# Optimization experiments

Hardware: AMD Instinct MI355X
Metric: run time of the kernel (lower is better)

The kernel has to match this reference:

```python
import jax, jax.numpy as jnp
import numpy as np

N_NODES = 100000
N_EDGES = 1600000
IN_F, HID, EMB = 128, 64, 32


def setup_inputs() -> dict:
    key = jax.random.key(0)
    ks = jax.random.split(key, 10)
    x = jax.random.normal(ks[0], (N_NODES, IN_F), dtype=jnp.float32)
    edge_index = jax.random.randint(ks[1], (2, N_EDGES), 0, N_NODES, dtype=jnp.int64)
    s = lambda k, sh, fan_in: jax.random.normal(k, sh, dtype=jnp.float32) / jnp.sqrt(jnp.float32(fan_in))
    return {
        "x": x,
        "edge_index": edge_index,
        # SAGEConv1: lin_l (applied to aggregated neighbors, with bias) + lin_r (root, no bias)
        "W1_l": s(ks[2], (IN_F, HID), IN_F), "b1": jnp.zeros((HID,), jnp.float32), "W1_r": s(ks[3], (IN_F, HID), IN_F),
        # SAGEConv2
        "W2_l": s(ks[4], (HID, EMB), HID), "b2": jnp.zeros((EMB,), jnp.float32), "W2_r": s(ks[5], (HID, EMB), HID),
        # risk head
        "Wh": s(ks[6], (EMB, 1), EMB), "bh": jnp.zeros((1,), jnp.float32),
    }


def _sage_conv(x, src, dst, W_l, b, W_r):
    # gather messages from source nodes, segment-mean at destination nodes
    msg_sum = jax.ops.segment_sum(x[src], dst, num_segments=N_NODES)  # [N, F]
    cnt = jax.ops.segment_sum(jnp.ones((src.shape[0],), x.dtype), dst, num_segments=N_NODES)
    mean_agg = msg_sum / jnp.maximum(cnt, 1.0)[:, None]  # isolated nodes -> 0
    return mean_agg @ W_l + b + x @ W_r


def reference(x, edge_index, W1_l, b1, W1_r, W2_l, b2, W2_r, Wh, bh):
    src, dst = edge_index[0], edge_index[1]
    h = jax.nn.relu(_sage_conv(x, src, dst, W1_l, b1, W1_r))
    # dropout is identity in eval mode
    embeddings = jax.nn.relu(_sage_conv(h, src, dst, W2_l, b2, W2_r))
    risk_scores = embeddings @ Wh + bh
    return embeddings, risk_scores
```

## Files before the change

### kernel.cpp

```cpp
#include <hip/hip_runtime.h>
#include <hip/hip_bf16.h>

#define N_NODES 100000
#define N_EDGES 1600000
#define NBUCK   196
#define BSHIFT  9
#define BCAP    12288

typedef __bf16 bf16x8 __attribute__((ext_vector_type(8)));
typedef float  f32x4  __attribute__((ext_vector_type(4)));
typedef float  f32x2  __attribute__((ext_vector_type(2)));


__device__ inline unsigned char enc_fp8(float v) {
    return (unsigned char)(__builtin_amdgcn_cvt_pk_fp8_f32(v, v, 0, 0) & 0xFF);
}

__global__ __launch_bounds__(256) void partition_k(const int* __restrict__ ei,
                                                   int* __restrict__ gcur,
                                                   unsigned* __restrict__ bbuf) {
    __shared__ int hist[NBUCK];
    __shared__ int cur[NBUCK];
    int t = threadIdx.x;
    for (int i = t; i < NBUCK; i += 256) hist[i] = 0;
    __syncthreads();
    int base = blockIdx.x * 4096;
    unsigned pk[16];
    int bk[16];
#pragma unroll
    for (int i = 0; i < 16; ++i) {
        int e = base + t + i * 256;
        if (e < N_EDGES) {
            int s = ei[e], d = ei[N_EDGES + e];
            int b = d >> BSHIFT;
            pk[i] = ((unsigned)(d & 511) << 17) | (unsigned)s;
            bk[i] = b;
            atomicAdd(&hist[b], 1);
        } else bk[i] = -1;
    }
    __syncthreads();
    for (int i = t; i < NBUCK; i += 256)
        cur[i] = atomicAdd(&gcur[i], hist[i]);
    __syncthreads();
#pragma unroll
    for (int i = 0; i < 16; ++i) {
        if (bk[i] >= 0) {
            int pos = atomicAdd(&cur[bk[i]], 1);
            bbuf[(size_t)bk[i] * BCAP + pos] = pk[i];
        }
    }
}

__global__ __launch_bounds__(256) void bucketcsr_k(const unsigned* __restrict__ bbuf,
                                                   const int* __restrict__ gcur,
                                                   int* __restrict__ cnt,
                                                   int* __restrict__ offsets,
                                                   int* __restrict__ csr) {
    __shared__ int lcnt[512];
    __shared__ int loff[512];
    __shared__ int lcur[512];
    __shared__ int ssum[256];
    int b = blockIdx.x, t = threadIdx.x;
    int m = gcur[b];
    const unsigned* src = bbuf + (size_t)b * BCAP;
    for (int i = t; i < 512; i += 256) lcnt[i] = 0;
    __syncthreads();
    for (int i = t; i < m; i += 256) atomicAdd(&lcnt[src[i] >> 17], 1);
    __syncthreads();
    int a0 = lcnt[2 * t], a1 = lcnt[2 * t + 1];
    ssum[t] = a0 + a1;
    __syncthreads();
    for (int off = 1; off < 256; off <<= 1) {
        int v = (t >= off) ? ssum[t - off] : 0;
        __syncthreads();
        ssum[t] += v;
        __syncthreads();
    }
    int ebase = (t == 0) ? 0 : ssum[t - 1];
    loff[2 * t] = ebase;
    loff[2 * t + 1] = ebase + a0;
    __syncthreads();
    for (int i = t; i < 512; i += 256) lcur[i] = loff[i];
    int nbase = b << BSHIFT;
    for (int i = t; i < 512; i += 256) {
        int n = nbase + i;
        if (n < N_NODES) {
            cnt[n] = lcnt[i];
            offsets[n] = b * BCAP + loff[i];
        }
    }
    __syncthreads();
    for (int i = t; i < m; i += 256) {
        unsigned p = src[i];
        int pos = atomicAdd(&lcur[p >> 17], 1);
        csr[(size_t)b * BCAP + pos] = (int)(p & 0x1FFFF);
    }
}

__global__ __launch_bounds__(256) void gemm1_k(const float* __restrict__ x,
                                               const float* __restrict__ W1l,
                                               const float* __restrict__ W1r,
                                               unsigned char* __restrict__ c1l,
                                               __bf16* __restrict__ c1r) {
    __shared__ __bf16 Bt[128 * 136];
    int tid = threadIdx.x;
    for (int idx = tid; idx < 8192; idx += 256) {
        int k = idx >> 6, n = idx & 63;
        Bt[n * 136 + k]        = (__bf16)W1l[idx];
        Bt[(n + 64) * 136 + k] = (__bf16)W1r[idx];
    }
    __syncthreads();

    int lane = tid & 63, wave = tid >> 6;
    int mbase = blockIdx.x * 64 + wave * 16;
    int col  = lane & 15;
    int kgrp = (lane >> 4) << 3;
    int mrow = mbase + col;
    int mclamp = mrow < N_NODES ? mrow : N_NODES - 1;
    const float* arow = x + (size_t)mclamp * 128;

    f32x4 acc[8];
#pragma unroll
    for (int i = 0; i < 8; ++i) acc[i] = (f32x4){0.f, 0.f, 0.f, 0.f};

#pragma unroll
    for (int ks = 0; ks < 4; ++ks) {
        int kk = ks * 32 + kgrp;
        f32x4 a0 = *(const f32x4*)(arow + kk);
        f32x4 a1 = *(const f32x4*)(arow + kk + 4);
        bf16x8 a;
#pragma unroll
        for (int i = 0; i < 4; ++i) { a[i] = (__bf16)a0[i]; a[i + 4] = (__bf16)a1[i]; }
#pragma unroll
        for (int nt = 0; nt < 8; ++nt) {
            bf16x8 b = *(const bf16x8*)(Bt + (nt * 16 + col) * 136 + kk);
            acc[nt] = __builtin_amdgcn_mfma_f32_16x16x32_bf16(a, b, acc[nt], 0, 0, 0);
        }
    }

    int r0 = mbase + ((lane >> 4) << 2);
#pragma unroll
    for (int r = 0; r < 4; ++r) {
        int m = r0 + r;
        if (m < N_NODES) {
#pragma unroll
            for (int nt = 0; nt < 4; ++nt)
                c1l[(size_t)m * 64 + nt * 16 + col] = enc_fp8(acc[nt][r]);
#pragma unroll
            for (int nt = 4; nt < 8; ++nt)
                c1r[(size_t)m * 64 + (nt - 4) * 16 + col] = (__bf16)acc[nt][r];
        }
    }
}

__global__ __launch_bounds__(256) void agg1_k(const unsigned char* __restrict__ c1l,
                                              const __bf16* __restrict__ c1r,
                                              const int* __restrict__ offsets,
                                              const int* __restrict__ cnt,
                                              const int* __restrict__ csr,
                                              const float* __restrict__ b1,
                                              __bf16* __restrict__ h) {
    int wave = blockIdx.x * 4 + (threadIdx.x >> 6);
    int lane = threadIdx.x & 63;
    int g = lane >> 3;
    int n = wave * 8 + g;
    int f8b = (lane & 7) << 3;
    int beg = offsets[n], deg = cnt[n];
    int end = beg + deg;
    float sum[8];
#pragma unroll
    for (int j = 0; j < 8; ++j) sum[j] = 0.f;
    for (int e = beg; e < end; e += 4) {
#pragma unroll
        for (int u = 0; u < 4; ++u) {
            int i = e + u;
            if (i < end) {
                int s = csr[i];
                uint2 w = *(const uint2*)(c1l + (size_t)s * 64 + f8b);
                f32x2 p0 = __builtin_amdgcn_cvt_pk_f32_fp8(w.x, 0);
                f32x2 p1 = __builtin_amdgcn_cvt_pk_f32_fp8(w.x, 1);
                f32x2 p2 = __builtin_amdgcn_cvt_pk_f32_fp8(w.y, 0);
                f32x2 p3 = __builtin_amdgcn_cvt_pk_f32_fp8(w.y, 1);
                sum[0] += p0[0]; sum[1] += p0[1];
                sum[2] += p1[0]; sum[3] += p1[1];
                sum[4] += p2[0]; sum[5] += p2[1];
                sum[6] += p3[0]; sum[7] += p3[1];
            }
        }
    }
    float cf = deg > 0 ? (float)deg : 1.f;
    bf16x8 rv = *(const bf16x8*)(c1r + (size_t)n * 64 + f8b);
    bf16x8 o;
#pragma unroll
    for (int j = 0; j < 8; ++j) {
        float v = sum[j] / cf + (float)rv[j] + b1[f8b + j];
        o[j] = (__bf16)(v > 0.f ? v : 0.f);
    }
    *(bf16x8*)(h + (size_t)n * 64 + f8b) = o;
}

__global__ __launch_bounds__(256) void gemm2_k(const __bf16* __restrict__ h,
                                               const float* __restrict__ W2l,
                                               const float* __restrict__ W2r,
                                               unsigned char* __restrict__ c2l,
                                               float* __restrict__ c2r) {
    __shared__ __bf16 Bt[64 * 72];
    int tid = threadIdx.x;
    for (int idx = tid; idx < 2048; idx += 256) {
        int k = idx >> 5, n = idx & 31;
        Bt[n * 72 + k]        = (__bf16)W2l[idx];
        Bt[(n + 32) * 72 + k] = (__bf16)W2r[idx];
    }
    __syncthreads();

    int lane = tid & 63, wave = tid >> 6;
    int mbase = blockIdx.x * 64 + wave * 16;
    int col  = lane & 15;
    int kgrp = (lane >> 4) << 3;
    int mrow = mbase + col;
    int mclamp = mrow < N_NODES ? mrow : N_NODES - 1;
    const __bf16* arow = h + (size_t)mclamp * 64;

    f32x4 acc[4];
#pragma unroll
    for (int i = 0; i < 4; ++i) acc[i] = (f32x4){0.f, 0.f, 0.f, 0.f};

#pragma unroll
    for (int ks = 0; ks < 2; ++ks) {
        int kk = ks * 32 + kgrp;
        bf16x8 a = *(const bf16x8*)(arow + kk);
#pragma unroll
        for (int nt = 0; nt < 4; ++nt) {
            bf16x8 b = *(const bf16x8*)(Bt + (nt * 16 + col) * 72 + kk);
            acc[nt] = __builtin_amdgcn_mfma_f32_16x16x32_bf16(a, b, acc[nt], 0, 0, 0);
        }
    }

    int r0 = mbase + ((lane >> 4) << 2);
#pragma unroll
    for (int r = 0; r < 4; ++r) {
        int m = r0 + r;
        if (m < N_NODES) {
#pragma unroll
            for (int nt = 0; nt < 2; ++nt)
                c2l[(size_t)m * 32 + nt * 16 + col] = enc_fp8(acc[nt][r]);
#pragma unroll
            for (int nt = 2; nt < 4; ++nt)
                c2r[(size_t)m * 32 + (nt - 2) * 16 + col] = acc[nt][r];
        }
    }
}

__global__ __launch_bounds__(256) void agg2_k(const unsigned char* __restrict__ c2l,
                                              const float* __restrict__ c2r,
                                              const int* __restrict__ offsets,
                                              const int* __restrict__ cnt,
                                              const int* __restrict__ csr,
                                              const float* __restrict__ b2,
                                              const float* __restrict__ Wh,
                                              const float* __restrict__ bh,
                                              float* __restrict__ out) {
    int wave = blockIdx.x * 4 + (threadIdx.x >> 6);
    int lane = threadIdx.x & 63;
    int g = lane >> 2;
    int n = wave * 16 + g;
    int f8b = (lane & 3) << 3;
    bool valid = n < N_NODES;
    int beg = 0, deg = 0;
    if (valid) { beg = offsets[n]; deg = cnt[n]; }
    int end = beg + deg;
    float sum[8];
#pragma unroll
    for (int j = 0; j < 8; ++j) sum[j] = 0.f;
    for (int e = beg; e < end; e += 4) {
#pragma unroll
        for (int u = 0; u < 4; ++u) {
            int i = e + u;
            if (i < end) {
                int s = csr[i];
                uint2 w = *(const uint2*)(c2l + (size_t)s * 32 + f8b);
                f32x2 p0 = __builtin_amdgcn_cvt_pk_f32_fp8(w.x, 0);
                f32x2 p1 = __builtin_amdgcn_cvt_pk_f32_fp8(w.x, 1);
                f32x2 p2 = __builtin_amdgcn_cvt_pk_f32_fp8(w.y, 0);
                f32x2 p3 = __builtin_amdgcn_cvt_pk_f32_fp8(w.y, 1);
                sum[0] += p0[0]; sum[1] += p0[1];
                sum[2] += p1[0]; sum[3] += p1[1];
                sum[4] += p2[0]; sum[5] += p2[1];
                sum[6] += p3[0]; sum[7] += p3[1];
            }
        }
    }
    float cf = deg > 0 ? (float)deg : 1.f;
    float r = 0.f;
    f32x4 o0, o1;
    if (valid) {
#pragma unroll
        for (int j = 0; j < 8; ++j) {
            float v = sum[j] / cf + c2r[(size_t)n * 32 + f8b + j] + b2[f8b + j];
            v = v > 0.f ? v : 0.f;
            if (j < 4) o0[j] = v; else o1[j - 4] = v;
            r += v * Wh[f8b + j];
        }
        *(f32x4*)(out + (size_t)n * 32 + f8b) = o0;
        *(f32x4*)(out + (size_t)n * 32 + f8b + 4) = o1;
    }
    r += __shfl_xor(r, 1, 64);
    r += __shfl_xor(r, 2, 64);
    if (valid && (lane & 3) == 0)
        out[(size_t)N_NODES * 32 + n] = r + bh[0];
}

extern "C" void kernel_launch(void* const* d_in, const int* in_sizes, int n_in,
                              void* d_out, int out_size, void* d_ws, size_t ws_size,
                              hipStream_t stream) {
    const float* x   = (const float*)d_in[0];
    const int*   ei  = (const int*)d_in[1];
    const float* W1l = (const float*)d_in[2];
    const float* b1  = (const float*)d_in[3];
    const float* W1r = (const float*)d_in[4];
    const float* W2l = (const float*)d_in[5];
    const float* b2  = (const float*)d_in[6];
    const float* W2r = (const float*)d_in[7];
    const float* Wh  = (const float*)d_in[8];
    const float* bh  = (const float*)d_in[9];
    float* out = (float*)d_out;

    char* ws = (char*)d_ws;
    unsigned char* c1l = (unsigned char*)(ws);
    __bf16*   c1r     = (__bf16*)(ws + 6400000);
    __bf16*   h       = (__bf16*)(ws + 19200000);
    unsigned char* c2l = (unsigned char*)(ws + 32000000);
    float*    c2r     = (float*)(ws + 35200000);
    int*      cnt     = (int*)(ws + 48000000);
    int*      offsets = (int*)(ws + 48400000);
    int*      gcur    = (int*)(ws + 48800000);
    unsigned* bbuf    = (unsigned*)(ws + 48804096);
    int*      csr     = (int*)(ws + 58437888);

    hipMemsetAsync(gcur, 0, NBUCK * 4, stream);

    partition_k<<<391, 256, 0, stream>>>(ei, gcur, bbuf);
    bucketcsr_k<<<NBUCK, 256, 0, stream>>>(bbuf, gcur, cnt, offsets, csr);
    gemm1_k    <<<1563, 256, 0, stream>>>(x, W1l, W1r, c1l, c1r);
    agg1_k     <<<3125, 256, 0, stream>>>(c1l, c1r, offsets, cnt, csr, b1, h);
    gemm2_k    <<<1563, 256, 0, stream>>>(h, W2l, W2r, c2l, c2r);
    agg2_k     <<<1563, 256, 0, stream>>>(c2l, c2r, offsets, cnt, csr, b2, Wh, bh, out);
}
```

Before: 237.2 us.

## Align CSR segments to 4 and batch 8 neighbor gathers per iteration

Pads each node's CSR segment start to a multiple of four so index lists can be read with aligned int4 loads. Both aggregation kernels now fetch eight neighbor indices at once and issue eight independent feature gathers before accumulating, which raises memory-level parallelism. Root-feature, c2r and Wh loads are hoisted ahead of the loop to overlap with it. The padding slightly grows bucket usage within BCAP. The int4 reads can also pull indices past a segment's end, but those lanes are masked out.

```diff
diff --git a/kernel.cpp b/kernel.cpp
--- a/kernel.cpp
+++ b/kernel.cpp
@@ -68,7 +68,8 @@
     for (int i = t; i < m; i += 256) atomicAdd(&lcnt[src[i] >> 17], 1);
     __syncthreads();
     int a0 = lcnt[2 * t], a1 = lcnt[2 * t + 1];
-    ssum[t] = a0 + a1;
+    int p0 = (a0 + 3) & ~3, p1 = (a1 + 3) & ~3;
+    ssum[t] = p0 + p1;
     __syncthreads();
     for (int off = 1; off < 256; off <<= 1) {
         int v = (t >= off) ? ssum[t - off] : 0;
@@ -78,7 +79,7 @@
     }
     int ebase = (t == 0) ? 0 : ssum[t - 1];
     loff[2 * t] = ebase;
-    loff[2 * t + 1] = ebase + a0;
+    loff[2 * t + 1] = ebase + p0;
     __syncthreads();
     for (int i = t; i < 512; i += 256) lcur[i] = loff[i];
     int nbase = b << BSHIFT;
@@ -167,29 +168,35 @@
     int f8b = (lane & 7) << 3;
     int beg = offsets[n], deg = cnt[n];
     int end = beg + deg;
+    bf16x8 rv = *(const bf16x8*)(c1r + (size_t)n * 64 + f8b);
+    const int4* csr4 = (const int4*)csr;
     float sum[8];
 #pragma unroll
     for (int j = 0; j < 8; ++j) sum[j] = 0.f;
-    for (int e = beg; e < end; e += 4) {
-#pragma unroll
-        for (int u = 0; u < 4; ++u) {
-            int i = e + u;
-            if (i < end) {
-                int s = csr[i];
-                uint2 w = *(const uint2*)(c1l + (size_t)s * 64 + f8b);
-                f32x2 p0 = __builtin_amdgcn_cvt_pk_f32_fp8(w.x, 0);
-                f32x2 p1 = __builtin_amdgcn_cvt_pk_f32_fp8(w.x, 1);
-                f32x2 p2 = __builtin_amdgcn_cvt_pk_f32_fp8(w.y, 0);
-                f32x2 p3 = __builtin_amdgcn_cvt_pk_f32_fp8(w.y, 1);
-                sum[0] += p0[0]; sum[1] += p0[1];
-                sum[2] += p1[0]; sum[3] += p1[1];
-                sum[4] += p2[0]; sum[5] += p2[1];
-                sum[6] += p3[0]; sum[7] += p3[1];
-            }
+    for (int e = beg; e < end; e += 8) {
+        int4 i0 = csr4[e >> 2];
+        int4 i1 = csr4[(e >> 2) + 1];
+        int sidx[8] = {i0.x, i0.y, i0.z, i0.w, i1.x, i1.y, i1.z, i1.w};
+        uint2 w[8];
+#pragma unroll
+        for (int u = 0; u < 8; ++u) {
+            w[u].x = 0u; w[u].y = 0u;
+            if (e + u < end)
+                w[u] = *(const uint2*)(c1l + (size_t)sidx[u] * 64 + f8b);
+        }
+#pragma unroll
+        for (int u = 0; u < 8; ++u) {
+            f32x2 p0 = __builtin_amdgcn_cvt_pk_f32_fp8(w[u].x, 0);
+            f32x2 p1 = __builtin_amdgcn_cvt_pk_f32_fp8(w[u].x, 1);
+            f32x2 p2 = __builtin_amdgcn_cvt_pk_f32_fp8(w[u].y, 0);
+            f32x2 p3 = __builtin_amdgcn_cvt_pk_f32_fp8(w[u].y, 1);
+            sum[0] += p0[0]; sum[1] += p0[1];
+            sum[2] += p1[0]; sum[3] += p1[1];
+            sum[4] += p2[0]; sum[5] += p2[1];
+            sum[6] += p3[0]; sum[7] += p3[1];
         }
     }
     float cf = deg > 0 ? (float)deg : 1.f;
-    bf16x8 rv = *(const bf16x8*)(c1r + (size_t)n * 64 + f8b);
     bf16x8 o;
 #pragma unroll
     for (int j = 0; j < 8; ++j) {
@@ -266,41 +273,53 @@
     int n = wave * 16 + g;
     int f8b = (lane & 3) << 3;
     bool valid = n < N_NODES;
-    int beg = 0, deg = 0;
-    if (valid) { beg = offsets[n]; deg = cnt[n]; }
+    int nc = valid ? n : N_NODES - 1;
+    int beg = offsets[nc], deg = valid ? cnt[n] : 0;
     int end = beg + deg;
+    f32x4 rr0 = *(const f32x4*)(c2r + (size_t)nc * 32 + f8b);
+    f32x4 rr1 = *(const f32x4*)(c2r + (size_t)nc * 32 + f8b + 4);
+    f32x4 wh0 = *(const f32x4*)(Wh + f8b);
+    f32x4 wh1 = *(const f32x4*)(Wh + f8b + 4);
+    const int4* csr4 = (const int4*)csr;
     float sum[8];
 #pragma unroll
     for (int j = 0; j < 8; ++j) sum[j] = 0.f;
-    for (int e = beg; e < end; e += 4) {
-#pragma unroll
-        for (int u = 0; u < 4; ++u) {
-            int i = e + u;
-            if (i < end) {
-                int s = csr[i];
-                uint2 w = *(const uint2*)(c2l + (size_t)s * 32 + f8b);
-                f32x2 p0 = __builtin_amdgcn_cvt_pk_f32_fp8(w.x, 0);
-                f32x2 p1 = __builtin_amdgcn_cvt_pk_f32_fp8(w.x, 1);
-                f32x2 p2 = __builtin_amdgcn_cvt_pk_f32_fp8(w.y, 0);
-                f32x2 p3 = __builtin_amdgcn_cvt_pk_f32_fp8(w.y, 1);
-                sum[0] += p0[0]; sum[1] += p0[1];
-                sum[2] += p1[0]; sum[3] += p1[1];
-                sum[4] += p2[0]; sum[5] += p2[1];
-                sum[6] += p3[0]; sum[7] += p3[1];
-            }
+    for (int e = beg; e < end; e += 8) {
+        int4 i0 = csr4[e >> 2];
+        int4 i1 = csr4[(e >> 2) + 1];
+        int sidx[8] = {i0.x, i0.y, i0.z, i0.w, i1.x, i1.y, i1.z, i1.w};
+        uint2 w[8];
+#pragma unroll
+        for (int u = 0; u < 8; ++u) {
+            w[u].x = 0u; w[u].y = 0u;
+            if (e + u < end)
+                w[u] = *(const uint2*)(c2l + (size_t)sidx[u] * 32 + f8b);
+        }
+#pragma unroll
+        for (int u = 0; u < 8; ++u) {
+            f32x2 p0 = __builtin_amdgcn_cvt_pk_f32_fp8(w[u].x, 0);
+            f32x2 p1 = __builtin_amdgcn_cvt_pk_f32_fp8(w[u].x, 1);
+            f32x2 p2 = __builtin_amdgcn_cvt_pk_f32_fp8(w[u].y, 0);
+            f32x2 p3 = __builtin_amdgcn_cvt_pk_f32_fp8(w[u].y, 1);
+            sum[0] += p0[0]; sum[1] += p0[1];
+            sum[2] += p1[0]; sum[3] += p1[1];
+            sum[4] += p2[0]; sum[5] += p2[1];
+            sum[6] += p3[0]; sum[7] += p3[1];
         }
     }
     float cf = deg > 0 ? (float)deg : 1.f;
     float r = 0.f;
     f32x4 o0, o1;
+#pragma unroll
+    for (int j = 0; j < 8; ++j) {
+        float root = (j < 4) ? rr0[j] : rr1[j - 4];
+        float whj  = (j < 4) ? wh0[j] : wh1[j - 4];
+        float v = sum[j] / cf + root + b2[f8b + j];
+        v = v > 0.f ? v : 0.f;
+        if (j < 4) o0[j] = v; else o1[j - 4] = v;
+        r += v * whj;
+    }
     if (valid) {
-#pragma unroll
-        for (int j = 0; j < 8; ++j) {
-            float v = sum[j] / cf + c2r[(size_t)n * 32 + f8b + j] + b2[f8b + j];
-            v = v > 0.f ? v : 0.f;
-            if (j < 4) o0[j] = v; else o1[j - 4] = v;
-            r += v * Wh[f8b + j];
-        }
         *(f32x4*)(out + (size_t)n * 32 + f8b) = o0;
         *(f32x4*)(out + (size_t)n * 32 + f8b + 4) = o1;
     }
```

New measurement: 221.0 us. 6.8% less time.
